# Kernel tuning notes

Measured on AMD Instinct MI355X. Metric: run time of the kernel, lower is better.

## Reference

```python
import jax, jax.numpy as jnp
import numpy as np

H, W = 8192, 16384          # dna_shape = (out_features, in_features)
NUM_TRANSFORMS = 8
NUM_POINTS = 1000           # hardcoded in source
CHAOS_ITERS = 10            # hardcoded in source
B = 2048


def setup_inputs() -> dict:
    key = jax.random.key(0)
    k1, k2, k3 = jax.random.split(key, 3)
    x = jax.random.normal(k1, (B, W), dtype=jnp.float32)
    # flat IFS params: [a,b,c,d,e,f,p] per transform; scaled down so affine maps are mostly contractive
    dna_params = jax.random.normal(k2, (NUM_TRANSFORMS * 7,), dtype=jnp.float32) * 0.5
    bias = jax.random.normal(k3, (H,), dtype=jnp.float32)
    return {"x": x, "dna_params": dna_params, "bias": bias}


def reference(x, dna_params, bias):
    params = dna_params.reshape(NUM_TRANSFORMS, 7)  # (T, 7)
    # theta[t] = [[a, b, e], [c, d, f]]  -> (T, 2, 3) affine maps
    theta = jnp.stack([
        jnp.stack([params[:, 0], params[:, 1], params[:, 4]], axis=1),
        jnp.stack([params[:, 2], params[:, 3], params[:, 5]], axis=1),
    ], axis=1)

    key = jax.random.key(1)
    kp, kg = jax.random.split(key)
    points = jax.random.uniform(kp, (NUM_POINTS, 2), dtype=x.dtype) * 2.0 - 1.0  # (N, 2) in [-1, 1)
    logits = jnp.broadcast_to(params[:, 6], (NUM_POINTS, NUM_TRANSFORMS))

    # Chaos game: 10 iterations of hard gumbel-softmax transform selection + affine map
    for i in range(CHAOS_ITERS):
        g = jax.random.gumbel(jax.random.fold_in(kg, i), (NUM_POINTS, NUM_TRANSFORMS), dtype=x.dtype)
        soft = jax.nn.softmax(logits + g, axis=-1)  # tau = 1.0
        hard = jax.nn.one_hot(jnp.argmax(soft, axis=-1), NUM_TRANSFORMS, dtype=soft.dtype)
        gw = hard + soft - jax.lax.stop_gradient(soft)          # straight-through hard sample (N, T)
        t_theta = jnp.einsum('nt,trc->nrc', gw, theta)          # (N, 2, 3) per-point affine
        ph = jnp.concatenate([points, jnp.ones((NUM_POINTS, 1), dtype=points.dtype)], axis=1)  # (N, 3)
        points = jnp.einsum('nrc,nc->nr', t_theta, ph)          # (N, 2)

    # Map attractor points to matrix coordinates
    y_coords = (points[:, 1] + 1.0) * 0.5 * (H - 1)
    x_coords = (points[:, 0] + 1.0) * 0.5 * (W - 1)
    y_low = jnp.clip(jnp.floor(y_coords).astype(jnp.int32), 0, H - 2)
    y_w = y_coords - y_low.astype(y_coords.dtype)
    x_low = jnp.clip(jnp.floor(x_coords).astype(jnp.int32), 0, W - 2)
    x_w = x_coords - x_low.astype(x_coords.dtype)

    # Bilinear gather along in_features: (B, N)
    x_vals = x[:, x_low] * (1.0 - x_w) + x[:, x_low + 1] * x_w

    # Bilinear scatter-add along out_features: (B, H)
    y = jnp.zeros((x.shape[0], H), dtype=x.dtype)
    y = y.at[:, y_low].add(x_vals * (1.0 - y_w))
    y = y.at[:, y_low + 1].add(x_vals * y_w)
    return y / NUM_POINTS + bias
```

## Files before the change

kernel.cpp:

```cpp
#include <hip/hip_runtime.h>
#include <stdint.h>

#ifndef PRNG_PARTITIONABLE
#define PRNG_PARTITIONABLE 1
#endif

namespace {

constexpr int kH  = 8192;
constexpr int kW  = 16384;
constexpr int kNT = 8;
constexpr int kNP = 1000;
constexpr int kCI = 10;
constexpr int kRPB = 2;

__device__ __forceinline__ uint32_t rotl32(uint32_t x, int n) {
  return (x << n) | (x >> (32 - n));
}

__device__ void threefry2x32(uint32_t k0, uint32_t k1, uint32_t c0, uint32_t c1,
                             uint32_t& o0, uint32_t& o1) {
  const uint32_t ks2 = k0 ^ k1 ^ 0x1BD11BDAu;
  uint32_t x0 = c0 + k0, x1 = c1 + k1;
#define TF_R(r) { x0 += x1; x1 = rotl32(x1, (r)); x1 ^= x0; }
  TF_R(13) TF_R(15) TF_R(26) TF_R(6)
  x0 += k1;  x1 += ks2 + 1u;
  TF_R(17) TF_R(29) TF_R(16) TF_R(24)
  x0 += ks2; x1 += k0 + 2u;
  TF_R(13) TF_R(15) TF_R(26) TF_R(6)
  x0 += k0;  x1 += k1 + 3u;
  TF_R(17) TF_R(29) TF_R(16) TF_R(24)
  x0 += k1;  x1 += ks2 + 4u;
  TF_R(13) TF_R(15) TF_R(26) TF_R(6)
  x0 += ks2; x1 += k0 + 5u;
#undef TF_R
  o0 = x0; o1 = x1;
}

__device__ __forceinline__ uint32_t random_bits32(uint32_t k0, uint32_t k1,
                                                  uint32_t i, uint32_t size) {
#if PRNG_PARTITIONABLE
  uint32_t o0, o1;
  threefry2x32(k0, k1, 0u , i, o0, o1);
  (void)size;
  return o0 ^ o1;
#else
  const uint32_t half = size / 2u;
  const uint32_t j = (i < half) ? i : (i - half);
  uint32_t o0, o1;
  threefry2x32(k0, k1, j, j + half, o0, o1);
  return (i < half) ? o0 : o1;
#endif
}

__device__ __forceinline__ float u01(uint32_t bits) {
  return __uint_as_float((bits >> 9) | 0x3f800000u) - 1.0f;
}

__device__ __forceinline__ int cvt_f32_i32_x86(float v) {
  if (!(v >= -2147483648.0f && v < 2147483648.0f)) return (int)0x80000000;
  return (int)v;
}

__global__ __launch_bounds__(256) void fractal_chaos(
    const float* __restrict__ dna, int4* __restrict__ rec) {
  const int gid  = blockIdx.x * blockDim.x + threadIdx.x;
  const int n    = gid >> 3;
  const int lane = gid & 7;
  if (n >= kNP) return;

  uint32_t kp0, kp1, kg0, kg1;
#if PRNG_PARTITIONABLE
  threefry2x32(0u, 1u, 0u, 0u, kp0, kp1);
  threefry2x32(0u, 1u, 0u, 1u, kg0, kg1);
#else
  uint32_t a0, a1, b0, b1;
  threefry2x32(0u, 1u, 0u, 2u, a0, a1);
  threefry2x32(0u, 1u, 1u, 3u, b0, b1);
  kp0 = a0; kp1 = b0; kg0 = a1; kg1 = b1;
#endif

  const float A  = dna[lane * 7 + 0], Bb = dna[lane * 7 + 1];
  const float C  = dna[lane * 7 + 2], D  = dna[lane * 7 + 3];
  const float E  = dna[lane * 7 + 4], F  = dna[lane * 7 + 5];
  const float P  = dna[lane * 7 + 6];

  float z[kCI];
  #pragma unroll
  for (int i = 0; i < kCI; ++i) {
    uint32_t ki0, ki1;
    threefry2x32(kg0, kg1, 0u, (uint32_t)i, ki0, ki1);
    const uint32_t bb = random_bits32(ki0, ki1, (uint32_t)(n * kNT + lane),
                                      (uint32_t)(kNP * kNT));
    const float u = fmaxf(u01(bb), 1.17549435e-38f);
    const float g = -logf(-logf(u));
    z[i] = P + g;
  }

  const uint32_t bx = random_bits32(kp0, kp1, (uint32_t)(2 * n),     2u * kNP);
  const uint32_t by = random_bits32(kp0, kp1, (uint32_t)(2 * n + 1), 2u * kNP);
  float px = u01(bx) * 2.0f - 1.0f;
  float py = u01(by) * 2.0f - 1.0f;

  #pragma unroll
  for (int i = 0; i < kCI; ++i) {
    float zb = z[i];
    int   bt = lane;
    #pragma unroll
    for (int m = 1; m < 8; m <<= 1) {
      const float zo = __shfl_xor(zb, m, 8);
      const int   to = __shfl_xor(bt, m, 8);
      if (zo > zb || (zo == zb && to < bt)) { zb = zo; bt = to; }
    }
    const float A_ = __shfl(A,  bt, 8), B_ = __shfl(Bb, bt, 8);
    const float C_ = __shfl(C,  bt, 8), D_ = __shfl(D,  bt, 8);
    const float E_ = __shfl(E,  bt, 8), F_ = __shfl(F,  bt, 8);
    const float nx = A_ * px + B_ * py + E_;
    const float ny = C_ * px + D_ * py + F_;
    px = nx; py = ny;
  }

  if (lane == 0) {
    const float xc = ((px + 1.0f) * 0.5f) * (float)(kW - 1);
    const float yc = ((py + 1.0f) * 0.5f) * (float)(kH - 1);
    int xl = cvt_f32_i32_x86(floorf(xc));
    int yl = cvt_f32_i32_x86(floorf(yc));
    xl = min(max(xl, 0), kW - 2);
    yl = min(max(yl, 0), kH - 2);
    const float xw = xc - (float)xl;
    const float yw = yc - (float)yl;
    rec[n] = make_int4(xl, __float_as_int(xw), yl, __float_as_int(yw));
  }
}

__global__ __launch_bounds__(1024) void fractal_apply(
    const float* __restrict__ x, const float* __restrict__ bias,
    const int4* __restrict__ rec, float* __restrict__ out, int B) {
  __shared__ __align__(16) float acc[kRPB * kH];
  const int b0 = blockIdx.x * kRPB;
  const int nrows = min(kRPB, B - b0);

  float4* acc4 = reinterpret_cast<float4*>(acc);
  constexpr int N4 = kRPB * kH / 4;
  for (int i = threadIdx.x; i < N4; i += 1024)
    acc4[i] = make_float4(0.f, 0.f, 0.f, 0.f);
  __syncthreads();

  if (threadIdx.x < kNP) {
    const int4 r = rec[threadIdx.x];
    const int   xl  = r.x;
    const float xw  = __int_as_float(r.y);
    const int   yl  = r.z;
    const float yw  = __int_as_float(r.w);
    const float xw0 = 1.0f - xw;
    const float w0  = 1.0f - yw;
    const float* xp = x + (size_t)b0 * kW + xl;
    #pragma unroll
    for (int rI = 0; rI < kRPB; ++rI) {
      if (rI < nrows) {
        const float xv = xp[(size_t)rI * kW] * xw0 + xp[(size_t)rI * kW + 1] * xw;
        atomicAdd(&acc[rI * kH + yl],     xv * w0);
        atomicAdd(&acc[rI * kH + yl + 1], xv * yw);
      }
    }
  }
  __syncthreads();

  const float4* __restrict__ bias4 = reinterpret_cast<const float4*>(bias);
  for (int i = threadIdx.x; i < N4; i += 1024) {
    const int row = i >> 11;
    const int col = i & 2047;
    if (row < nrows) {
      const float4 a  = acc4[i];
      const float4 bi = bias4[col];
      float4 o;
      o.x = a.x / 1000.0f + bi.x;
      o.y = a.y / 1000.0f + bi.y;
      o.z = a.z / 1000.0f + bi.z;
      o.w = a.w / 1000.0f + bi.w;
      reinterpret_cast<float4*>(out + (size_t)(b0 + row) * kH)[col] = o;
    }
  }
}

}

extern "C" void kernel_launch(void* const* d_in, const int* in_sizes, int n_in,
                              void* d_out, int out_size, void* d_ws, size_t ws_size,
                              hipStream_t stream) {
  const float* x    = (const float*)d_in[0];
  const float* dna  = (const float*)d_in[1];
  const float* bias = (const float*)d_in[2];
  float* out = (float*)d_out;
  int4* rec = (int4*)d_ws;

  const int chaosThreads = kNP * 8;
  fractal_chaos<<<(chaosThreads + 255) / 256, 256, 0, stream>>>(dna, rec);

  const int B = in_sizes[0] / kW;
  fractal_apply<<<(B + kRPB - 1) / kRPB, 1024, 0, stream>>>(x, bias, rec, out, B);
}
```

Before: 46.50 us.

## Stage input rows in shared memory with coalesced loads, one row per block

```diff
diff --git a/kernel.cpp b/kernel.cpp
--- a/kernel.cpp
+++ b/kernel.cpp
@@ -12,7 +12,8 @@
 constexpr int kNT = 8;
 constexpr int kNP = 1000;
 constexpr int kCI = 10;
-constexpr int kRPB = 2;
+
+typedef float floatx4 __attribute__((ext_vector_type(4)));
 
 __device__ __forceinline__ uint32_t rotl32(uint32_t x, int n) {
   return (x << n) | (x >> (32 - n));
@@ -135,51 +136,63 @@
 
 __global__ __launch_bounds__(1024) void fractal_apply(
     const float* __restrict__ x, const float* __restrict__ bias,
-    const int4* __restrict__ rec, float* __restrict__ out, int B) {
-  __shared__ __align__(16) float acc[kRPB * kH];
-  const int b0 = blockIdx.x * kRPB;
-  const int nrows = min(kRPB, B - b0);
+    const int4* __restrict__ rec, float* __restrict__ out) {
+  __shared__ __align__(16) float acc[kH];
+  __shared__ __align__(16) float xbuf[kW / 2];
+
+  const int b   = blockIdx.x;
+  const int tid = threadIdx.x;
 
   float4* acc4 = reinterpret_cast<float4*>(acc);
-  constexpr int N4 = kRPB * kH / 4;
-  for (int i = threadIdx.x; i < N4; i += 1024)
-    acc4[i] = make_float4(0.f, 0.f, 0.f, 0.f);
-  __syncthreads();
-
-  if (threadIdx.x < kNP) {
-    const int4 r = rec[threadIdx.x];
-    const int   xl  = r.x;
-    const float xw  = __int_as_float(r.y);
-    const int   yl  = r.z;
-    const float yw  = __int_as_float(r.w);
-    const float xw0 = 1.0f - xw;
-    const float w0  = 1.0f - yw;
-    const float* xp = x + (size_t)b0 * kW + xl;
-    #pragma unroll
-    for (int rI = 0; rI < kRPB; ++rI) {
-      if (rI < nrows) {
-        const float xv = xp[(size_t)rI * kW] * xw0 + xp[(size_t)rI * kW + 1] * xw;
-        atomicAdd(&acc[rI * kH + yl],     xv * w0);
-        atomicAdd(&acc[rI * kH + yl + 1], xv * yw);
-      }
+  acc4[tid]        = make_float4(0.f, 0.f, 0.f, 0.f);
+  acc4[tid + 1024] = make_float4(0.f, 0.f, 0.f, 0.f);
+
+  const bool havept = tid < kNP;
+  int xl = 0, yl = 0;
+  float xw = 0.f, yw = 0.f, xw0 = 0.f, w0 = 0.f;
+  if (havept) {
+    const int4 r = rec[tid];
+    xl = r.x; xw = __int_as_float(r.y);
+    yl = r.z; yw = __int_as_float(r.w);
+    xw0 = 1.0f - xw; w0 = 1.0f - yw;
+  }
+
+  const float* __restrict__ xrow = x + (size_t)b * kW;
+  float4* xbuf4 = reinterpret_cast<float4*>(xbuf);
+
+  #pragma unroll
+  for (int p = 0; p < 2; ++p) {
+    const float4* __restrict__ src =
+        reinterpret_cast<const float4*>(xrow + p * (kW / 2));
+    xbuf4[tid]        = src[tid];
+    xbuf4[tid + 1024] = src[tid + 1024];
+    __syncthreads();
+
+    if (havept && (xl >> 13) == p) {
+      const int loc = xl & (kW / 2 - 1);
+      const float v0 = xbuf[loc];
+      const float v1 = (loc < kW / 2 - 1) ? xbuf[loc + 1] : xrow[xl + 1];
+      const float xv = v0 * xw0 + v1 * xw;
+      atomicAdd(&acc[yl],     xv * w0);
+      atomicAdd(&acc[yl + 1], xv * yw);
     }
-  }
-  __syncthreads();
+    __syncthreads();
+  }
 
   const float4* __restrict__ bias4 = reinterpret_cast<const float4*>(bias);
-  for (int i = threadIdx.x; i < N4; i += 1024) {
-    const int row = i >> 11;
-    const int col = i & 2047;
-    if (row < nrows) {
-      const float4 a  = acc4[i];
-      const float4 bi = bias4[col];
-      float4 o;
-      o.x = a.x / 1000.0f + bi.x;
-      o.y = a.y / 1000.0f + bi.y;
-      o.z = a.z / 1000.0f + bi.z;
-      o.w = a.w / 1000.0f + bi.w;
-      reinterpret_cast<float4*>(out + (size_t)(b0 + row) * kH)[col] = o;
-    }
+  floatx4* __restrict__ out4 =
+      reinterpret_cast<floatx4*>(out + (size_t)b * kH);
+  #pragma unroll
+  for (int i = 0; i < 2; ++i) {
+    const int idx = tid + i * 1024;
+    const float4 a  = acc4[idx];
+    const float4 bi = bias4[idx];
+    floatx4 o;
+    o.x = a.x / 1000.0f + bi.x;
+    o.y = a.y / 1000.0f + bi.y;
+    o.z = a.z / 1000.0f + bi.z;
+    o.w = a.w / 1000.0f + bi.w;
+    __builtin_nontemporal_store(o, &out4[idx]);
   }
 }
 
@@ -198,5 +211,5 @@
   fractal_chaos<<<(chaosThreads + 255) / 256, 256, 0, stream>>>(dna, rec);
 
   const int B = in_sizes[0] / kW;
-  fractal_apply<<<(B + kRPB - 1) / kRPB, 1024, 0, stream>>>(x, bias, rec, out, B);
-}
+  fractal_apply<<<B, 1024, 0, stream>>>(x, bias, rec, out);
+}
```

Measured after the change: 50.52 us. 1.09x slower.

## Sort sample points by column bucket and prefetch gathers before smem zeroing

Applied to the files above, without the earlier changes.

```diff
diff --git a/kernel.cpp b/kernel.cpp
--- a/kernel.cpp
+++ b/kernel.cpp
@@ -13,6 +13,11 @@
 constexpr int kNP = 1000;
 constexpr int kCI = 10;
 constexpr int kRPB = 2;
+
+constexpr size_t kOffRec  = 0;
+constexpr size_t kOffRec2 = 16384;
+
+typedef float floatx4 __attribute__((ext_vector_type(4)));
 
 __device__ __forceinline__ uint32_t rotl32(uint32_t x, int n) {
   return (x << n) | (x >> (32 - n));
@@ -133,32 +138,82 @@
   }
 }
 
+__global__ __launch_bounds__(1024) void fractal_build(
+    const int4* __restrict__ rec, int4* __restrict__ rec2) {
+  __shared__ uint32_t cnt[1024];
+  __shared__ uint32_t seg[1024];
+
+  const int t = threadIdx.x;
+  cnt[t] = 0;
+  __syncthreads();
+
+  int4 r = make_int4(0, 0, 0, 0);
+  int bx = 0;
+  const bool hav = t < kNP;
+  if (hav) {
+    r = rec[t];
+    bx = r.x >> 4;
+    atomicAdd(&cnt[bx], 1u);
+  }
+  __syncthreads();
+
+  seg[t] = cnt[t];
+  __syncthreads();
+  #pragma unroll
+  for (int o = 1; o < 1024; o <<= 1) {
+    uint32_t v = (t >= o) ? seg[t - o] : 0u;
+    __syncthreads();
+    seg[t] += v;
+    __syncthreads();
+  }
+  cnt[t] = (t > 0) ? seg[t - 1] : 0u;
+  __syncthreads();
+
+  if (hav) {
+    const uint32_t p = atomicAdd(&cnt[bx], 1u);
+    rec2[p] = r;
+  }
+}
+
 __global__ __launch_bounds__(1024) void fractal_apply(
     const float* __restrict__ x, const float* __restrict__ bias,
-    const int4* __restrict__ rec, float* __restrict__ out, int B) {
+    const int4* __restrict__ rec2, float* __restrict__ out, int B) {
   __shared__ __align__(16) float acc[kRPB * kH];
   const int b0 = blockIdx.x * kRPB;
   const int nrows = min(kRPB, B - b0);
-
-  float4* acc4 = reinterpret_cast<float4*>(acc);
-  constexpr int N4 = kRPB * kH / 4;
-  for (int i = threadIdx.x; i < N4; i += 1024)
-    acc4[i] = make_float4(0.f, 0.f, 0.f, 0.f);
-  __syncthreads();
-
-  if (threadIdx.x < kNP) {
-    const int4 r = rec[threadIdx.x];
-    const int   xl  = r.x;
-    const float xw  = __int_as_float(r.y);
-    const int   yl  = r.z;
-    const float yw  = __int_as_float(r.w);
-    const float xw0 = 1.0f - xw;
-    const float w0  = 1.0f - yw;
-    const float* xp = x + (size_t)b0 * kW + xl;
+  const int tid = threadIdx.x;
+
+  const bool havept = tid < kNP;
+  int4 r = make_int4(0, 0, 0, 0);
+  float v0[kRPB], v1[kRPB];
+  if (havept) {
+    r = rec2[tid];
+    const float* xp = x + (size_t)b0 * kW + r.x;
     #pragma unroll
     for (int rI = 0; rI < kRPB; ++rI) {
       if (rI < nrows) {
-        const float xv = xp[(size_t)rI * kW] * xw0 + xp[(size_t)rI * kW + 1] * xw;
+        v0[rI] = xp[(size_t)rI * kW];
+        v1[rI] = xp[(size_t)rI * kW + 1];
+      }
+    }
+  }
+
+  float4* acc4 = reinterpret_cast<float4*>(acc);
+  constexpr int N4 = kRPB * kH / 4;
+  for (int i = tid; i < N4; i += 1024)
+    acc4[i] = make_float4(0.f, 0.f, 0.f, 0.f);
+  __syncthreads();
+
+  if (havept) {
+    const float xw = __int_as_float(r.y);
+    const float yw = __int_as_float(r.w);
+    const float xw0 = 1.0f - xw;
+    const float w0  = 1.0f - yw;
+    const int yl = r.z;
+    #pragma unroll
+    for (int rI = 0; rI < kRPB; ++rI) {
+      if (rI < nrows) {
+        const float xv = v0[rI] * xw0 + v1[rI] * xw;
         atomicAdd(&acc[rI * kH + yl],     xv * w0);
         atomicAdd(&acc[rI * kH + yl + 1], xv * yw);
       }
@@ -166,19 +221,20 @@
   }
   __syncthreads();
 
-  const float4* __restrict__ bias4 = reinterpret_cast<const float4*>(bias);
-  for (int i = threadIdx.x; i < N4; i += 1024) {
+  const floatx4* __restrict__ bias4 = reinterpret_cast<const floatx4*>(bias);
+  for (int i = tid; i < N4; i += 1024) {
     const int row = i >> 11;
     const int col = i & 2047;
     if (row < nrows) {
       const float4 a  = acc4[i];
-      const float4 bi = bias4[col];
-      float4 o;
+      const floatx4 bi = bias4[col];
+      floatx4 o;
       o.x = a.x / 1000.0f + bi.x;
       o.y = a.y / 1000.0f + bi.y;
       o.z = a.z / 1000.0f + bi.z;
       o.w = a.w / 1000.0f + bi.w;
-      reinterpret_cast<float4*>(out + (size_t)(b0 + row) * kH)[col] = o;
+      floatx4* dst = reinterpret_cast<floatx4*>(out + (size_t)(b0 + row) * kH);
+      __builtin_nontemporal_store(o, &dst[col]);
     }
   }
 }
@@ -192,11 +248,15 @@
   const float* dna  = (const float*)d_in[1];
   const float* bias = (const float*)d_in[2];
   float* out = (float*)d_out;
-  int4* rec = (int4*)d_ws;
-
-  const int chaosThreads = kNP * 8;
-  fractal_chaos<<<(chaosThreads + 255) / 256, 256, 0, stream>>>(dna, rec);
+
+  char* ws = (char*)d_ws;
+  int4* rec  = (int4*)(ws + kOffRec);
+  int4* rec2 = (int4*)(ws + kOffRec2);
+
+  fractal_chaos<<<(kNP * 8 + 255) / 256, 256, 0, stream>>>(dna, rec);
+  fractal_build<<<1, 1024, 0, stream>>>(rec, rec2);
 
   const int B = in_sizes[0] / kW;
-  fractal_apply<<<(B + kRPB - 1) / kRPB, 1024, 0, stream>>>(x, bias, rec, out, B);
-}
+  fractal_apply<<<(B + kRPB - 1) / kRPB, 1024, 0, stream>>>(x, bias, rec2,
+                                                            out, B);
+}
```

After: 49.22 us. 5.8% more time.
